# Optimization experiments

Hardware: AMD Instinct MI355X
Metric: run time of the kernel (lower is better)

The kernel has to match this reference:

```python
import jax, jax.numpy as jnp
import numpy as np

GRID_DIMS = (64, 64, 64)
GRID_LOWER = np.array([0.0, 0.0, 0.0], np.float32)
GRID_STEPS = np.array([0.015625, 0.015625, 0.015625], np.float32)
RADIUS = 0.03125
STENCIL = 2  # ceil(radius / step)


def _poly6(d2, h):
    # standard SPH poly6 smoothing kernel: 315/(64 pi h^9) (h^2 - d^2)^3, d <= h
    c = np.float32(315.0 / (64.0 * np.pi * h ** 9))
    return jnp.where(d2 <= h * h, c * (h * h - d2) ** 3, 0.0)


def particles2grid(locs, data, density):
    # locs [B,N,3], data [B,N,C], density [B,N] -> grid [B,X,Y,Z,C]
    B, N, _ = locs.shape
    C = data.shape[-1]
    X, Y, Z = GRID_DIMS
    dims = jnp.array(GRID_DIMS, jnp.int32)
    r = jnp.arange(-STENCIL, STENCIL + 1)
    offs = jnp.stack(jnp.meshgrid(r, r, r, indexing='ij'), -1).reshape(-1, 3)  # [K,3]
    base = jnp.floor((locs - GRID_LOWER) / GRID_STEPS).astype(jnp.int32)        # [B,N,3]
    cells = base[:, :, None, :] + offs                                          # [B,N,K,3]
    centers = GRID_LOWER + (cells.astype(locs.dtype) + 0.5) * GRID_STEPS
    d2 = jnp.sum((centers - locs[:, :, None, :]) ** 2, -1)                      # [B,N,K]
    w = _poly6(d2, RADIUS)
    w = jnp.where(jnp.all((cells >= 0) & (cells < dims), -1), w, 0.0)
    contrib = w[..., None] * (data / density[..., None])[:, :, None, :]         # [B,N,K,C]
    cells = jnp.clip(cells, 0, dims - 1)
    flat = (cells[..., 0] * Y + cells[..., 1]) * Z + cells[..., 2]              # [B,N,K]

    def splat(f, c):
        return jnp.zeros((X * Y * Z, C), data.dtype).at[f.reshape(-1)].add(c.reshape(-1, C))

    return jax.vmap(splat)(flat, contrib).reshape(B, X, Y, Z, C)


def grid2particles(grid, locs):
    # trilinear interpolation of grid [B,X,Y,Z,C] at particle locations [B,N,3]
    B, X, Y, Z, C = grid.shape
    dims = jnp.array([X, Y, Z], jnp.int32)
    pos = (locs - GRID_LOWER) / GRID_STEPS - 0.5                                # cell-center coords
    i0 = jnp.floor(pos).astype(jnp.int32)
    frac = pos - i0.astype(locs.dtype)
    gflat = grid.reshape(B, X * Y * Z, C)
    gather = jax.vmap(lambda g, f: g[f])                                        # [B,N] -> [B,N,C]
    out = jnp.zeros((B, locs.shape[1], C), grid.dtype)
    for dx in (0, 1):
        for dy in (0, 1):
            for dz in (0, 1):
                off = jnp.array([dx, dy, dz], jnp.int32)
                idx = i0 + off
                wd = jnp.where(off == 1, frac, 1.0 - frac)                      # [B,N,3]
                w = wd[..., 0] * wd[..., 1] * wd[..., 2]
                w = jnp.where(jnp.all((idx >= 0) & (idx < dims), -1), w, 0.0)
                idx = jnp.clip(idx, 0, dims - 1)
                flat = (idx[..., 0] * Y + idx[..., 1]) * Z + idx[..., 2]
                out = out + w[..., None] * gather(gflat, flat)
    return out


def conv3d(x, w, b):
    y = jax.lax.conv_general_dilated(x, w, (1, 1, 1), 'SAME',
                                     dimension_numbers=('NCDHW', 'OIDHW', 'NCDHW'))
    return y + b[None, :, None, None, None]


def prelu(x, a):
    return jnp.where(x >= 0, x, a * x)


def setup_inputs() -> dict:
    key = jax.random.key(0)
    ks = jax.random.split(key, 8)
    B, N = 2, 32768
    Cin, K, Cout = 4, 32, 4
    s = lambda fan: np.float32(1.0 / np.sqrt(fan * 27))
    return {
        'locs': jax.random.uniform(ks[0], (B, N, 3), jnp.float32),
        'data': jax.random.normal(ks[1], (B, N, Cin), jnp.float32),
        'density': jax.random.uniform(ks[2], (B, N), jnp.float32, 0.5, 1.5),
        'W0': jax.random.normal(ks[3], (K, Cin, 3, 3, 3), jnp.float32) * s(Cin),
        'b0': jnp.zeros((K,), jnp.float32),
        'W1': jax.random.normal(ks[4], (K, K, 3, 3, 3), jnp.float32) * s(K),
        'b1': jnp.zeros((K,), jnp.float32),
        'W2': jax.random.normal(ks[5], (K, K, 3, 3, 3), jnp.float32) * s(K),
        'b2': jnp.zeros((K,), jnp.float32),
        'W3': jax.random.normal(ks[6], (Cout, K, 3, 3, 3), jnp.float32) * s(K),
        'b3': jnp.zeros((Cout,), jnp.float32),
        'a0': jnp.full((1,), 0.25, jnp.float32),
        'a1': jnp.full((1,), 0.25, jnp.float32),
        'a2': jnp.full((1,), 0.25, jnp.float32),
    }


def reference(locs, data, density, W0, b0, W1, b1, W2, b2, W3, b3, a0, a1, a2):
    grid = particles2grid(locs, data, density)            # [B,X,Y,Z,Cin]
    g = jnp.transpose(grid, (0, 4, 1, 2, 3))              # NCDHW
    g = prelu(conv3d(g, W0, b0), a0)
    g = prelu(conv3d(g, W1, b1), a1)
    g = prelu(conv3d(g, W2, b2), a2)
    g = conv3d(g, W3, b3)
    g = jnp.transpose(g, (0, 2, 3, 4, 1))                 # [B,X,Y,Z,Cout]
    return grid2particles(g, locs)                        # [B,N,Cout]
```

## Files before the change

### kernel.cpp

```cpp
#include <hip/hip_runtime.h>

#define BATCH 2
#define NPART 32768
#define GD 64
#define NVOX (BATCH * GD * GD * GD)

typedef unsigned short ushortT;
typedef __attribute__((ext_vector_type(8))) short short8;
typedef __attribute__((ext_vector_type(16))) float float16;

__device__ __forceinline__ float poly6_c() {
    const double H9 = 1.0 / 35184372088832.0;
    return (float)(315.0 / (64.0 * 3.14159265358979323846 * H9));
}

__device__ __forceinline__ ushortT bf16_rne(float f) {
    unsigned int u = __float_as_uint(f);
    u = (u + 0x7fffu + ((u >> 16) & 1u)) >> 16;
    return (ushortT)u;
}

__device__ __forceinline__ int imax(int a, int b) { return a > b ? a : b; }
__device__ __forceinline__ int imin(int a, int b) { return a < b ? a : b; }

__device__ __forceinline__ void load_lds16(const void* g, void* l) {
    __builtin_amdgcn_global_load_lds(
        (const __attribute__((address_space(1))) void*)g,
        (__attribute__((address_space(3))) void*)l, 16, 0, 0);
}

__global__ void zero_ints_kernel(int* __restrict__ p, int n) {
    int t = blockIdx.x * blockDim.x + threadIdx.x;
    if (t < n) p[t] = 0;
}

__global__ __launch_bounds__(256) void bin_count_kernel(
    const float* __restrict__ locs, int* __restrict__ counts) {
    int t = blockIdx.x * blockDim.x + threadIdx.x;
    if (t >= BATCH * NPART) return;
    int b = t >> 15;
    int bx = ((int)floorf(locs[t * 3 + 0] * 64.0f)) >> 1;
    int by = ((int)floorf(locs[t * 3 + 1] * 64.0f)) >> 1;
    int bz = ((int)floorf(locs[t * 3 + 2] * 64.0f)) >> 1;
    atomicAdd(&counts[b * 32768 + ((bx * 32) + by) * 32 + bz], 1);
}

__global__ __launch_bounds__(256) void scanA_kernel(
    const int* __restrict__ counts, int* __restrict__ offsets,
    int* __restrict__ blockSum) {
    __shared__ int sh[256];
    int tid = threadIdx.x, g = blockIdx.x;
    int v = counts[g * 256 + tid];
    sh[tid] = v;
    __syncthreads();
    for (int off = 1; off < 256; off <<= 1) {
        int u = (tid >= off) ? sh[tid - off] : 0;
        __syncthreads();
        sh[tid] += u;
        __syncthreads();
    }
    offsets[g * 256 + tid] = sh[tid] - v;
    if (tid == 255) blockSum[g] = sh[255];
}

__global__ __launch_bounds__(256) void scanB_kernel(
    int* __restrict__ offsets, const int* __restrict__ blockSum) {
    __shared__ int sh[256];
    int tid = threadIdx.x, g = blockIdx.x;
    sh[tid] = (tid < g) ? blockSum[tid] : 0;
    __syncthreads();
    for (int off = 128; off > 0; off >>= 1) {
        if (tid < off) sh[tid] += sh[tid + off];
        __syncthreads();
    }
    offsets[g * 256 + tid] += sh[0];
    if (g == 255 && tid == 255) offsets[65536] = BATCH * NPART;
}

__global__ __launch_bounds__(256) void bin_scatter_kernel(
    const float* __restrict__ locs, const float* __restrict__ data,
    const float* __restrict__ density, const int* __restrict__ offsets,
    int* __restrict__ cursor, float* __restrict__ payload) {
    int t = blockIdx.x * blockDim.x + threadIdx.x;
    if (t >= BATCH * NPART) return;
    int b = t >> 15;
    float px = locs[t * 3 + 0];
    float py = locs[t * 3 + 1];
    float pz = locs[t * 3 + 2];
    int bx = ((int)floorf(px * 64.0f)) >> 1;
    int by = ((int)floorf(py * 64.0f)) >> 1;
    int bz = ((int)floorf(pz * 64.0f)) >> 1;
    int bb = b * 32768 + ((bx * 32) + by) * 32 + bz;
    int slot = atomicAdd(&cursor[bb], 1);
    int idx = offsets[bb] + slot;
    float inv_d = 1.0f / density[t];
    float4 p0 = {px, py, pz, data[t * 4 + 0] * inv_d};
    float4 p1 = {data[t * 4 + 1] * inv_d, data[t * 4 + 2] * inv_d,
                 data[t * 4 + 3] * inv_d, 0.f};
    *(float4*)(payload + idx * 8)     = p0;
    *(float4*)(payload + idx * 8 + 4) = p1;
}

__global__ __launch_bounds__(256) void splat_gather_kernel(
    const float* __restrict__ payload, const int* __restrict__ offsets,
    ushortT* __restrict__ g8) {
    __shared__ float plist[256 * 8];
    __shared__ int segS[36];
    __shared__ int segP[37];
    __shared__ int shTot[1];

    int wg = blockIdx.x;
    int sb = wg & 511, b = wg >> 9;
    int X0 = (sb >> 6) * 8, Y0 = ((sb >> 3) & 7) * 8, Z0 = (sb & 7) * 8;
    int tid = threadIdx.x;

    int bxlo = imax(0, (X0 - 2) >> 1), bxhi = imin(31, (X0 + 9) >> 1);
    int bylo = imax(0, (Y0 - 2) >> 1), byhi = imin(31, (Y0 + 9) >> 1);
    int bzlo = imax(0, (Z0 - 2) >> 1), bzhi = imin(31, (Z0 + 9) >> 1);
    int ny = byhi - bylo + 1;
    int ns = (bxhi - bxlo + 1) * ny;
    if (tid < ns) {
        int bx = bxlo + tid / ny, by = bylo + tid % ny;
        int row = b * 32768 + (bx * 32 + by) * 32;
        int s = offsets[row + bzlo];
        int e = offsets[row + bzhi + 1];
        segS[tid] = s;
        segP[tid] = e - s;
    }
    __syncthreads();
    if (tid == 0) {
        int p = 0;
        for (int k = 0; k < ns; ++k) { int len = segP[k]; segP[k] = p; p += len; }
        segP[ns] = p;
        shTot[0] = p;
    }
    __syncthreads();

    const float step = 0.015625f;
    const float h2 = 0.03125f * 0.03125f;
    const float cc = poly6_c();
    int total = shTot[0];

    int l = tid & 63, w = tid >> 6;
    int cx = X0 + 4 * (w >> 1) + (l >> 4);
    int cy = Y0 + 4 * (w & 1) + ((l >> 2) & 3);
    int cz0 = Z0 + (l & 3);
    float xc  = ((float)cx  + 0.5f) * step;
    float yc  = ((float)cy  + 0.5f) * step;
    float zc0 = ((float)cz0 + 0.5f) * step;
    float zc1 = zc0 + 4.0f * step;

    float a00 = 0.f, a01 = 0.f, a02 = 0.f, a03 = 0.f;
    float a10 = 0.f, a11 = 0.f, a12 = 0.f, a13 = 0.f;

    int nchunks = (total + 255) >> 8;
    for (int ch = 0; ch < nchunks; ++ch) {
        __syncthreads();
        int jj = (ch << 8) + tid;
        if (jj < total) {
            int k = 0;
            while (jj >= segP[k + 1]) ++k;
            int idx = segS[k] + (jj - segP[k]);
            *(float4*)(plist + tid * 8)     = *(const float4*)(payload + idx * 8);
            *(float4*)(plist + tid * 8 + 4) = *(const float4*)(payload + idx * 8 + 4);
        }
        __syncthreads();
        int cnt = imin(256, total - (ch << 8));
        for (int p = 0; p < cnt; ++p) {
            float4 pa = *(const float4*)(plist + p * 8);
            float dx = pa.x - xc, dy = pa.y - yc;
            float dxy2 = fmaf(dy, dy, dx * dx);
            if (!__any(dxy2 <= h2)) continue;
            float4 pv = *(const float4*)(plist + p * 8 + 4);
            float dz0 = pa.z - zc0;
            float d20 = fmaf(dz0, dz0, dxy2);
            float u0 = fmaxf(h2 - d20, 0.f);
            float w0 = (cc * u0) * (u0 * u0);
            a00 = fmaf(w0, pa.w, a00);
            a01 = fmaf(w0, pv.x, a01);
            a02 = fmaf(w0, pv.y, a02);
            a03 = fmaf(w0, pv.z, a03);
            float dz1 = pa.z - zc1;
            float d21 = fmaf(dz1, dz1, dxy2);
            float u1 = fmaxf(h2 - d21, 0.f);
            float w1 = (cc * u1) * (u1 * u1);
            a10 = fmaf(w1, pa.w, a10);
            a11 = fmaf(w1, pv.x, a11);
            a12 = fmaf(w1, pv.y, a12);
            a13 = fmaf(w1, pv.z, a13);
        }
    }

    size_t cellBase = (size_t)(((b * 64 + cx) * 64 + cy) * 64);
    short8 o;
    o[0] = (short)bf16_rne(a00); o[1] = (short)bf16_rne(a01);
    o[2] = (short)bf16_rne(a02); o[3] = (short)bf16_rne(a03);
    o[4] = 0; o[5] = 0; o[6] = 0; o[7] = 0;
    *(short8*)(g8 + (cellBase + cz0) * 8) = o;
    o[0] = (short)bf16_rne(a10); o[1] = (short)bf16_rne(a11);
    o[2] = (short)bf16_rne(a12); o[3] = (short)bf16_rne(a13);
    *(short8*)(g8 + (cellBase + cz0 + 4) * 8) = o;
}

__global__ void repack_all_kernel(
    const float* __restrict__ W0, const float* __restrict__ W1,
    const float* __restrict__ W2, const float* __restrict__ W3,
    short* __restrict__ Bp) {
    int t = blockIdx.x * blockDim.x + threadIdx.x;
    if (t >= 176 * 512) return;
    int kt = t >> 9;
    const float* W; int O, I, CINP, ktL;
    if (kt < 14)       { W = W0; O = 32; I = 4;  CINP = 8;  ktL = kt; }
    else if (kt < 68)  { W = W1; O = 32; I = 32; CINP = 32; ktL = kt - 14; }
    else if (kt < 122) { W = W2; O = 32; I = 32; CINP = 32; ktL = kt - 68; }
    else               { W = W3; O = 4;  I = 32; CINP = 32; ktL = kt - 122; }
    int l = (t >> 3) & 63, j = t & 7;
    int n = l & 31, q = l >> 5;
    int k = ktL * 16 + 8 * q + j;
    int tap = k / CINP;
    int ic  = k - tap * CINP;
    float v = 0.f;
    if (tap < 27 && ic < I && n < O) v = W[(n * I + ic) * 27 + tap];
    Bp[t] = (short)bf16_rne(v);
}

template <int ICG, int KT, bool FINAL>
__global__ __launch_bounds__(256, 3) void mfma_conv_kernel(
    const ushortT* __restrict__ in, const short* __restrict__ Bpack,
    const float* __restrict__ bias, const float* __restrict__ alpha,
    const float* __restrict__ zguard, void* __restrict__ outv) {
    constexpr int CIN = ICG * 8;
    constexpr int NCH = 24 * ICG * 34;
    __shared__ short lds[NCH * 8];
    int wg = ((blockIdx.x & 7) << 8) | (blockIdx.x >> 3);
    int zh = wg & 1, yq = (wg >> 1) & 15, xp = (wg >> 5) & 31, b = wg >> 10;
    int X0 = xp * 2, Y0 = yq * 4, Z0 = zh * 32;
    int tid = threadIdx.x;

    const ushortT* inb = in + (size_t)b * (64 * 64 * 64 * CIN);
#pragma unroll
    for (int it = 0; it < (NCH + 255) / 256; ++it) {
        int ccid = it * 256 + tid;
        if (ccid < NCH) {
            int col = ccid / (ICG * 34);
            int rem = ccid - col * (ICG * 34);
            int icg = rem / 34;
            int zi  = rem - icg * 34;
            int gx = X0 + col / 6 - 1;
            int gy = Y0 + col % 6 - 1;
            int gz = Z0 + zi - 1;
            const void* src = (const void*)zguard;
            if ((unsigned)gx < 64u && (unsigned)gy < 64u && (unsigned)gz < 64u)
                src = (const void*)(inb + ((size_t)(((gx * 64) + gy) * 64 + gz)) * CIN + icg * 8);
            load_lds16(src, (void*)(lds + ccid * 8));
        }
    }
    __syncthreads();

    int l = tid & 63, w = tid >> 6;
    int wx = w >> 1;
    int cyA = (w & 1) * 2, cyB = cyA + 1;
    int n = l & 31, q = l >> 5;

    float bval = FINAL ? (n < 4 ? bias[n] : 0.f) : bias[n];
    float16 accA, accB;
#pragma unroll
    for (int r = 0; r < 16; ++r) { accA[r] = bval; accB[r] = bval; }

    const short* bp = Bpack + (size_t)l * 8;
    int laneZ = (l & 31) * 8;

    short8 bf[4];
#pragma unroll
    for (int i = 0; i < 4; ++i) bf[i] = *(const short8*)(bp + i * 512);

#pragma unroll
    for (int kt = 0; kt < KT; ++kt) {
        short8 bcur = bf[kt & 3];
        if (kt + 4 < KT) bf[kt & 3] = *(const short8*)(bp + (kt + 4) * 512);
        int aofsA, aofsB;
        if constexpr (ICG == 1) {
            int tap0 = kt * 2, tap1 = kt * 2 + 1;
            if (tap1 > 26) tap1 = 26;
            int dx0 = tap0 / 9, r0 = tap0 - dx0 * 9, dy0 = r0 / 3, dz0 = r0 - dy0 * 3;
            int dx1 = tap1 / 9, r1 = tap1 - dx1 * 9, dy1 = r1 / 3, dz1 = r1 - dy1 * 3;
            int cA0 = (((wx + dx0) * 6 + (cyA + dy0)) * 34 + dz0) * 8;
            int cA1 = (((wx + dx1) * 6 + (cyA + dy1)) * 34 + dz1) * 8;
            int cB0 = (((wx + dx0) * 6 + (cyB + dy0)) * 34 + dz0) * 8;
            int cB1 = (((wx + dx1) * 6 + (cyB + dy1)) * 34 + dz1) * 8;
            aofsA = q ? cA1 : cA0;
            aofsB = q ? cB1 : cB0;
        } else {
            int tap = kt >> 1;
            int dx = tap / 9, rr = tap - dx * 9, dy = rr / 3, dz = rr - dy * 3;
            int icg = (kt & 1) * 2 + q;
            aofsA = ((((wx + dx) * 6 + (cyA + dy)) * ICG + icg) * 34 + dz) * 8;
            aofsB = ((((wx + dx) * 6 + (cyB + dy)) * ICG + icg) * 34 + dz) * 8;
        }
        short8 afragA = *(const short8*)(lds + aofsA + laneZ);
        short8 afragB = *(const short8*)(lds + aofsB + laneZ);
        accA = __builtin_amdgcn_mfma_f32_32x32x16_bf16(afragA, bcur, accA, 0, 0, 0);
        accB = __builtin_amdgcn_mfma_f32_32x32x16_bf16(afragB, bcur, accB, 0, 0, 0);
    }

    size_t baseA = (size_t)(((b * 64 + X0 + wx) * 64 + (Y0 + cyA)) * 64) + Z0;
    size_t baseB = (size_t)(((b * 64 + X0 + wx) * 64 + (Y0 + cyB)) * 64) + Z0;
    if (FINAL) {
        float* out = (float*)outv;
        if (n < 4) {
#pragma unroll
            for (int r = 0; r < 16; ++r) {
                int z = (r & 3) + 8 * (r >> 2) + 4 * q;
                out[(baseA + z) * 4 + n] = accA[r];
                out[(baseB + z) * 4 + n] = accB[r];
            }
        }
    } else {
        float a = alpha[0];
        ushortT* out = (ushortT*)outv;
#pragma unroll
        for (int r = 0; r < 16; ++r) {
            int z = (r & 3) + 8 * (r >> 2) + 4 * q;
            float vA = accA[r];
            vA = vA >= 0.f ? vA : a * vA;
            out[(baseA + z) * 32 + n] = bf16_rne(vA);
            float vB = accB[r];
            vB = vB >= 0.f ? vB : a * vB;
            out[(baseB + z) * 32 + n] = bf16_rne(vB);
        }
    }
}

__global__ __launch_bounds__(256) void gather_kernel(
    const float* __restrict__ grid, const float* __restrict__ locs,
    float* __restrict__ out) {
    int t = blockIdx.x * blockDim.x + threadIdx.x;
    if (t >= BATCH * NPART) return;
    int b = t >> 15;

    float px = locs[t * 3 + 0] * 64.0f - 0.5f;
    float py = locs[t * 3 + 1] * 64.0f - 0.5f;
    float pz = locs[t * 3 + 2] * 64.0f - 0.5f;
    int ix = (int)floorf(px);
    int iy = (int)floorf(py);
    int iz = (int)floorf(pz);
    float fx = px - (float)ix;
    float fy = py - (float)iy;
    float fz = pz - (float)iz;

    const float* gb = grid + (size_t)b * GD * GD * GD * 4;
    float o0 = 0.f, o1 = 0.f, o2 = 0.f, o3 = 0.f;

#pragma unroll
    for (int dx = 0; dx < 2; ++dx) {
        int x = ix + dx;
        if ((unsigned)x > 63u) continue;
        float wx = dx ? fx : 1.0f - fx;
#pragma unroll
        for (int dy = 0; dy < 2; ++dy) {
            int y = iy + dy;
            if ((unsigned)y > 63u) continue;
            float wy = dy ? fy : 1.0f - fy;
#pragma unroll
            for (int dz = 0; dz < 2; ++dz) {
                int z = iz + dz;
                if ((unsigned)z > 63u) continue;
                float wz = dz ? fz : 1.0f - fz;
                float w = wx * wy * wz;
                const float4 g = *(const float4*)(gb + (size_t)(((x * GD) + y) * GD + z) * 4);
                o0 += w * g.x; o1 += w * g.y; o2 += w * g.z; o3 += w * g.w;
            }
        }
    }
    out[t * 4 + 0] = o0;
    out[t * 4 + 1] = o1;
    out[t * 4 + 2] = o2;
    out[t * 4 + 3] = o3;
}

extern "C" void kernel_launch(void* const* d_in, const int* in_sizes, int n_in,
                              void* d_out, int out_size, void* d_ws, size_t ws_size,
                              hipStream_t stream) {
    const float* locs    = (const float*)d_in[0];
    const float* data    = (const float*)d_in[1];
    const float* density = (const float*)d_in[2];
    const float* W0 = (const float*)d_in[3];
    const float* b0 = (const float*)d_in[4];
    const float* W1 = (const float*)d_in[5];
    const float* b1 = (const float*)d_in[6];
    const float* W2 = (const float*)d_in[7];
    const float* b2 = (const float*)d_in[8];
    const float* W3 = (const float*)d_in[9];
    const float* b3 = (const float*)d_in[10];
    const float* a0 = (const float*)d_in[11];
    const float* a1 = (const float*)d_in[12];
    const float* a2 = (const float*)d_in[13];
    float* out = (float*)d_out;

    char* ws = (char*)d_ws;
    ushortT* g8  = (ushortT*)(ws);
    ushortT* gA  = (ushortT*)(ws + 8388608);
    ushortT* gB  = (ushortT*)(ws + 41943040);
    float*  gF   = (float*)(ws + 75497472);
    short*  Bp   = (short*)(ws + 83886080);
    short*  Bp0  = Bp;
    short*  Bp1  = Bp + 14 * 512;
    short*  Bp2  = Bp + 68 * 512;
    short*  Bp3  = Bp + 122 * 512;
    float* zguard   = (float*)(ws + 84066240);
    int*   counts   = (int*)(ws + 84066304);
    int*   cursor   = (int*)(ws + 84328448);
    int*   offsets  = (int*)(ws + 84590592);
    int*   blockSum = (int*)(ws + 84852752);
    float* payload  = (float*)(ws + 84853888);

    zero_ints_kernel<<<(131088 + 255) / 256, 256, 0, stream>>>((int*)zguard, 131088);
    bin_count_kernel<<<(BATCH * NPART) / 256, 256, 0, stream>>>(locs, counts);
    scanA_kernel<<<256, 256, 0, stream>>>(counts, offsets, blockSum);
    scanB_kernel<<<256, 256, 0, stream>>>(offsets, blockSum);
    bin_scatter_kernel<<<(BATCH * NPART) / 256, 256, 0, stream>>>(
        locs, data, density, offsets, cursor, payload);

    repack_all_kernel<<<(176 * 512 + 255) / 256, 256, 0, stream>>>(W0, W1, W2, W3, Bp);

    splat_gather_kernel<<<BATCH * 512, 256, 0, stream>>>(payload, offsets, g8);

    const int CGRID = 2048;
    mfma_conv_kernel< 1, 14, false><<<CGRID, 256, 0, stream>>>(g8, Bp0, b0, a0, zguard, gA);
    mfma_conv_kernel< 4, 54, false><<<CGRID, 256, 0, stream>>>(gA, Bp1, b1, a1, zguard, gB);
    mfma_conv_kernel< 4, 54, false><<<CGRID, 256, 0, stream>>>(gB, Bp2, b2, a2, zguard, gA);
    mfma_conv_kernel< 4, 54, true ><<<CGRID, 256, 0, stream>>>(gA, Bp3, b3, b3, zguard, gF);

    gather_kernel<<<(BATCH * NPART) / 256, 256, 0, stream>>>(gF, locs, out);
}
```

Baseline: 247.5 us.

## Enlarge conv tile to 4x4 columns per block and merge prep kernels

Each conv workgroup now covers 4 x-slices by 4 y-rows, up from 2 by 4. Each wave computes four 32x32 MFMA accumulators that share one B fragment per k-step, and the block grid is halved. This raises reuse of the LDS halo, since 6x6 columns now feed 16 outputs instead of 4x6 feeding 8, and it amortizes the B-fragment loads. The cost is more accumulator registers and LDS per block, and the occupancy hint drops from 3 to 2. Separately, the zero-fill and weight-repack kernels are merged into one launch to save launch overhead.

```diff
diff --git a/kernel.cpp b/kernel.cpp
--- a/kernel.cpp
+++ b/kernel.cpp
@@ -29,9 +29,33 @@
         (__attribute__((address_space(3))) void*)l, 16, 0, 0);
 }
 
-__global__ void zero_ints_kernel(int* __restrict__ p, int n) {
-    int t = blockIdx.x * blockDim.x + threadIdx.x;
-    if (t < n) p[t] = 0;
+__global__ __launch_bounds__(256) void prep_kernel(
+    int* __restrict__ zp,
+    const float* __restrict__ W0, const float* __restrict__ W1,
+    const float* __restrict__ W2, const float* __restrict__ W3,
+    short* __restrict__ Bp) {
+    int bid = blockIdx.x, tid = threadIdx.x;
+    if (bid < 513) {
+        int t = bid * 256 + tid;
+        if (t < 131088) zp[t] = 0;
+        return;
+    }
+    int t = (bid - 513) * 256 + tid;
+    if (t >= 176 * 512) return;
+    int kt = t >> 9;
+    const float* W; int O, I, CINP, ktL;
+    if (kt < 14)       { W = W0; O = 32; I = 4;  CINP = 8;  ktL = kt; }
+    else if (kt < 68)  { W = W1; O = 32; I = 32; CINP = 32; ktL = kt - 14; }
+    else if (kt < 122) { W = W2; O = 32; I = 32; CINP = 32; ktL = kt - 68; }
+    else               { W = W3; O = 4;  I = 32; CINP = 32; ktL = kt - 122; }
+    int l = (t >> 3) & 63, j = t & 7;
+    int n = l & 31, q = l >> 5;
+    int k = ktL * 16 + 8 * q + j;
+    int tap = k / CINP;
+    int ic  = k - tap * CINP;
+    float v = 0.f;
+    if (tap < 27 && ic < I && n < O) v = W[(n * I + ic) * 27 + tap];
+    Bp[t] = (short)bf16_rne(v);
 }
 
 __global__ __launch_bounds__(256) void bin_count_kernel(
@@ -202,39 +226,17 @@
     *(short8*)(g8 + (cellBase + cz0 + 4) * 8) = o;
 }
 
-__global__ void repack_all_kernel(
-    const float* __restrict__ W0, const float* __restrict__ W1,
-    const float* __restrict__ W2, const float* __restrict__ W3,
-    short* __restrict__ Bp) {
-    int t = blockIdx.x * blockDim.x + threadIdx.x;
-    if (t >= 176 * 512) return;
-    int kt = t >> 9;
-    const float* W; int O, I, CINP, ktL;
-    if (kt < 14)       { W = W0; O = 32; I = 4;  CINP = 8;  ktL = kt; }
-    else if (kt < 68)  { W = W1; O = 32; I = 32; CINP = 32; ktL = kt - 14; }
-    else if (kt < 122) { W = W2; O = 32; I = 32; CINP = 32; ktL = kt - 68; }
-    else               { W = W3; O = 4;  I = 32; CINP = 32; ktL = kt - 122; }
-    int l = (t >> 3) & 63, j = t & 7;
-    int n = l & 31, q = l >> 5;
-    int k = ktL * 16 + 8 * q + j;
-    int tap = k / CINP;
-    int ic  = k - tap * CINP;
-    float v = 0.f;
-    if (tap < 27 && ic < I && n < O) v = W[(n * I + ic) * 27 + tap];
-    Bp[t] = (short)bf16_rne(v);
-}
-
 template <int ICG, int KT, bool FINAL>
-__global__ __launch_bounds__(256, 3) void mfma_conv_kernel(
+__global__ __launch_bounds__(256, 2) void mfma_conv_kernel(
     const ushortT* __restrict__ in, const short* __restrict__ Bpack,
     const float* __restrict__ bias, const float* __restrict__ alpha,
     const float* __restrict__ zguard, void* __restrict__ outv) {
     constexpr int CIN = ICG * 8;
-    constexpr int NCH = 24 * ICG * 34;
+    constexpr int NCH = 36 * ICG * 34;
     __shared__ short lds[NCH * 8];
-    int wg = ((blockIdx.x & 7) << 8) | (blockIdx.x >> 3);
-    int zh = wg & 1, yq = (wg >> 1) & 15, xp = (wg >> 5) & 31, b = wg >> 10;
-    int X0 = xp * 2, Y0 = yq * 4, Z0 = zh * 32;
+    int wg = ((blockIdx.x & 7) << 7) | (blockIdx.x >> 3);
+    int zh = wg & 1, yq = (wg >> 1) & 15, xp = (wg >> 5) & 15, b = wg >> 9;
+    int X0 = xp * 4, Y0 = yq * 4, Z0 = zh * 32;
     int tid = threadIdx.x;
 
     const ushortT* inb = in + (size_t)b * (64 * 64 * 64 * CIN);
@@ -258,14 +260,14 @@
     __syncthreads();
 
     int l = tid & 63, w = tid >> 6;
-    int wx = w >> 1;
-    int cyA = (w & 1) * 2, cyB = cyA + 1;
     int n = l & 31, q = l >> 5;
 
     float bval = FINAL ? (n < 4 ? bias[n] : 0.f) : bias[n];
-    float16 accA, accB;
-#pragma unroll
-    for (int r = 0; r < 16; ++r) { accA[r] = bval; accB[r] = bval; }
+    float16 acc0, acc1, acc2, acc3;
+#pragma unroll
+    for (int r = 0; r < 16; ++r) {
+        acc0[r] = bval; acc1[r] = bval; acc2[r] = bval; acc3[r] = bval;
+    }
 
     const short* bp = Bpack + (size_t)l * 8;
     int laneZ = (l & 31) * 8;
@@ -278,41 +280,45 @@
     for (int kt = 0; kt < KT; ++kt) {
         short8 bcur = bf[kt & 3];
         if (kt + 4 < KT) bf[kt & 3] = *(const short8*)(bp + (kt + 4) * 512);
-        int aofsA, aofsB;
+        int o0, o1, o2, o3;
         if constexpr (ICG == 1) {
             int tap0 = kt * 2, tap1 = kt * 2 + 1;
             if (tap1 > 26) tap1 = 26;
             int dx0 = tap0 / 9, r0 = tap0 - dx0 * 9, dy0 = r0 / 3, dz0 = r0 - dy0 * 3;
             int dx1 = tap1 / 9, r1 = tap1 - dx1 * 9, dy1 = r1 / 3, dz1 = r1 - dy1 * 3;
-            int cA0 = (((wx + dx0) * 6 + (cyA + dy0)) * 34 + dz0) * 8;
-            int cA1 = (((wx + dx1) * 6 + (cyA + dy1)) * 34 + dz1) * 8;
-            int cB0 = (((wx + dx0) * 6 + (cyB + dy0)) * 34 + dz0) * 8;
-            int cB1 = (((wx + dx1) * 6 + (cyB + dy1)) * 34 + dz1) * 8;
-            aofsA = q ? cA1 : cA0;
-            aofsB = q ? cB1 : cB0;
+#define AOFS1(c) (q ? ((((w + dx1) * 6 + ((c) + dy1)) * 34 + dz1) * 8) \
+                    : ((((w + dx0) * 6 + ((c) + dy0)) * 34 + dz0) * 8))
+            o0 = AOFS1(0); o1 = AOFS1(1); o2 = AOFS1(2); o3 = AOFS1(3);
+#undef AOFS1
         } else {
             int tap = kt >> 1;
             int dx = tap / 9, rr = tap - dx * 9, dy = rr / 3, dz = rr - dy * 3;
             int icg = (kt & 1) * 2 + q;
-            aofsA = ((((wx + dx) * 6 + (cyA + dy)) * ICG + icg) * 34 + dz) * 8;
-            aofsB = ((((wx + dx) * 6 + (cyB + dy)) * ICG + icg) * 34 + dz) * 8;
-        }
-        short8 afragA = *(const short8*)(lds + aofsA + laneZ);
-        short8 afragB = *(const short8*)(lds + aofsB + laneZ);
-        accA = __builtin_amdgcn_mfma_f32_32x32x16_bf16(afragA, bcur, accA, 0, 0, 0);
-        accB = __builtin_amdgcn_mfma_f32_32x32x16_bf16(afragB, bcur, accB, 0, 0, 0);
-    }
-
-    size_t baseA = (size_t)(((b * 64 + X0 + wx) * 64 + (Y0 + cyA)) * 64) + Z0;
-    size_t baseB = (size_t)(((b * 64 + X0 + wx) * 64 + (Y0 + cyB)) * 64) + Z0;
+#define AOFS4(c) (((((w + dx) * 6 + ((c) + dy)) * ICG + icg) * 34 + dz) * 8)
+            o0 = AOFS4(0); o1 = AOFS4(1); o2 = AOFS4(2); o3 = AOFS4(3);
+#undef AOFS4
+        }
+        short8 a0 = *(const short8*)(lds + o0 + laneZ);
+        short8 a1 = *(const short8*)(lds + o1 + laneZ);
+        short8 a2 = *(const short8*)(lds + o2 + laneZ);
+        short8 a3 = *(const short8*)(lds + o3 + laneZ);
+        acc0 = __builtin_amdgcn_mfma_f32_32x32x16_bf16(a0, bcur, acc0, 0, 0, 0);
+        acc1 = __builtin_amdgcn_mfma_f32_32x32x16_bf16(a1, bcur, acc1, 0, 0, 0);
+        acc2 = __builtin_amdgcn_mfma_f32_32x32x16_bf16(a2, bcur, acc2, 0, 0, 0);
+        acc3 = __builtin_amdgcn_mfma_f32_32x32x16_bf16(a3, bcur, acc3, 0, 0, 0);
+    }
+
+    size_t base0 = (size_t)(((b * 64 + X0 + w) * 64 + Y0) * 64) + Z0;
     if (FINAL) {
         float* out = (float*)outv;
         if (n < 4) {
 #pragma unroll
             for (int r = 0; r < 16; ++r) {
                 int z = (r & 3) + 8 * (r >> 2) + 4 * q;
-                out[(baseA + z) * 4 + n] = accA[r];
-                out[(baseB + z) * 4 + n] = accB[r];
+                out[(base0 + z) * 4 + n]        = acc0[r];
+                out[(base0 + 64 + z) * 4 + n]   = acc1[r];
+                out[(base0 + 128 + z) * 4 + n]  = acc2[r];
+                out[(base0 + 192 + z) * 4 + n]  = acc3[r];
             }
         }
     } else {
@@ -321,12 +327,14 @@
 #pragma unroll
         for (int r = 0; r < 16; ++r) {
             int z = (r & 3) + 8 * (r >> 2) + 4 * q;
-            float vA = accA[r];
-            vA = vA >= 0.f ? vA : a * vA;
-            out[(baseA + z) * 32 + n] = bf16_rne(vA);
-            float vB = accB[r];
-            vB = vB >= 0.f ? vB : a * vB;
-            out[(baseB + z) * 32 + n] = bf16_rne(vB);
+            float v0 = acc0[r]; v0 = v0 >= 0.f ? v0 : a * v0;
+            out[(base0 + z) * 32 + n] = bf16_rne(v0);
+            float v1 = acc1[r]; v1 = v1 >= 0.f ? v1 : a * v1;
+            out[(base0 + 64 + z) * 32 + n] = bf16_rne(v1);
+            float v2 = acc2[r]; v2 = v2 >= 0.f ? v2 : a * v2;
+            out[(base0 + 128 + z) * 32 + n] = bf16_rne(v2);
+            float v3 = acc3[r]; v3 = v3 >= 0.f ? v3 : a * v3;
+            out[(base0 + 192 + z) * 32 + n] = bf16_rne(v3);
         }
     }
 }
@@ -414,18 +422,17 @@
     int*   blockSum = (int*)(ws + 84852752);
     float* payload  = (float*)(ws + 84853888);
 
-    zero_ints_kernel<<<(131088 + 255) / 256, 256, 0, stream>>>((int*)zguard, 131088);
+    prep_kernel<<<513 + 352, 256, 0, stream>>>((int*)zguard, W0, W1, W2, W3, Bp);
+
     bin_count_kernel<<<(BATCH * NPART) / 256, 256, 0, stream>>>(locs, counts);
     scanA_kernel<<<256, 256, 0, stream>>>(counts, offsets, blockSum);
     scanB_kernel<<<256, 256, 0, stream>>>(offsets, blockSum);
     bin_scatter_kernel<<<(BATCH * NPART) / 256, 256, 0, stream>>>(
         locs, data, density, offsets, cursor, payload);
 
-    repack_all_kernel<<<(176 * 512 + 255) / 256, 256, 0, stream>>>(W0, W1, W2, W3, Bp);
-
     splat_gather_kernel<<<BATCH * 512, 256, 0, stream>>>(payload, offsets, g8);
 
-    const int CGRID = 2048;
+    const int CGRID = 1024;
     mfma_conv_kernel< 1, 14, false><<<CGRID, 256, 0, stream>>>(g8, Bp0, b0, a0, zguard, gA);
     mfma_conv_kernel< 4, 54, false><<<CGRID, 256, 0, stream>>>(gA, Bp1, b1, a1, zguard, gB);
     mfma_conv_kernel< 4, 54, false><<<CGRID, 256, 0, stream>>>(gB, Bp2, b2, a2, zguard, gA);
```

Result: no change. 248.9 us (+0.6%).
